# Kernel optimization log

Hardware: AMD Instinct MI355X
Metric: run time of the kernel (lower is better)

The kernel has to match this reference:

```python
import jax, jax.numpy as jnp
import numpy as np

TOP_K = 64
TEMPERATURE = 1.0
EPS = 1e-12  # torch F.normalize eps


def _normalize(v):
    # matches torch.nn.functional.normalize(v, dim=-1)
    n = jnp.linalg.norm(v, axis=-1, keepdims=True)
    return v / jnp.maximum(n, EPS)


def setup_inputs() -> dict:
    key = jax.random.key(0)
    k1, k2 = jax.random.split(key)
    x = jax.random.normal(k1, (4, 1024, 768), dtype=jnp.float32)
    codebook = jax.random.normal(k2, (8192, 768), dtype=jnp.float32)
    alpha = jnp.float32(0.5)
    return {"x": x, "codebook": codebook, "alpha": alpha}


def reference(x, codebook, alpha):
    K = TOP_K
    x_n = _normalize(x)                              # [B,T,D]
    cb_n = _normalize(codebook)                      # [N,D]
    sims = jnp.einsum('btd,nd->btn', x_n, cb_n)      # [B,T,N]
    activations = jax.nn.relu(sims)
    topk_vals, topk_idx = jax.lax.top_k(activations, K)  # [B,T,K]
    protos = codebook[topk_idx]                      # [B,T,K,D] gather
    protos_n = _normalize(protos)
    # per-token KxK pairwise similarity
    sim = jnp.einsum('btkd,btjd->btkj', protos_n, protos_n)
    sim = sim - jnp.eye(K, dtype=sim.dtype)
    sim = jax.nn.relu(sim)
    w = jax.nn.softmax(topk_vals / TEMPERATURE, axis=-1)  # [B,T,K]
    inhibition = jnp.einsum('btkj,btj->btk', sim, w)      # [B,T,K]
    result_topk = jax.nn.relu(topk_vals * (1.0 - alpha * inhibition))
    out = jnp.einsum('btk,btkd->btd', result_topk, protos)  # weighted sum
    return x + out
```

## Files before the change

kernel.cpp:

```cpp
#include <hip/hip_runtime.h>

#define TOKENS 4096
#define DIM    768
#define NCODE  8192
#define TOPK   64
#define CAP    512
#define LCAP   24
#define TAU    0.07f
#define NBIN   256
#define SELCAP 128
#define POOL   80
#define BLO    61
#define BHI    67

typedef __attribute__((ext_vector_type(4))) float          f32x4;
typedef __attribute__((ext_vector_type(8))) _Float16       half8;
typedef __attribute__((ext_vector_type(8))) unsigned short ushort8;

__device__ __forceinline__ unsigned short f2h(float f) {
  _Float16 h = (_Float16)f;
  return *(unsigned short*)&h;
}
__device__ __forceinline__ float h2f(unsigned short u) {
  _Float16 h = *(_Float16*)&u;
  return (float)h;
}

__device__ __forceinline__ int binof(float v) {
  int b = (int)((v - TAU) * (256.0f / 0.28f));
  return b < 0 ? 0 : (b > 255 ? 255 : b);
}

__device__ __forceinline__ void gload16(const unsigned short* g, unsigned short* l) {
  __builtin_amdgcn_global_load_lds((const __attribute__((address_space(1))) unsigned int*)g,
                                   (__attribute__((address_space(3))) unsigned int*)l,
                                   16, 0, 0);
}

__device__ __forceinline__ double dot12(const float4& xa, const float4& xb, const float4& xc,
                                        const float4& a, const float4& b, const float4& c) {
  double acc = (double)xa.x * (double)a.x;
  acc = fma((double)xa.y, (double)a.y, acc);
  acc = fma((double)xa.z, (double)a.z, acc);
  acc = fma((double)xa.w, (double)a.w, acc);
  acc = fma((double)xb.x, (double)b.x, acc);
  acc = fma((double)xb.y, (double)b.y, acc);
  acc = fma((double)xb.z, (double)b.z, acc);
  acc = fma((double)xb.w, (double)b.w, acc);
  acc = fma((double)xc.x, (double)c.x, acc);
  acc = fma((double)xc.y, (double)c.y, acc);
  acc = fma((double)xc.z, (double)c.z, acc);
  acc = fma((double)xc.w, (double)c.w, acc);
  return acc;
}

__global__ __launch_bounds__(256) void normcvt_kernel(const float* __restrict__ V,
                                                      unsigned short* __restrict__ Vn,
                                                      double* __restrict__ Rd) {
  int row = blockIdx.x, tid = threadIdx.x;
  const float* v = V + (size_t)row * DIM;
  float a = v[tid], b = v[tid + 256], c = v[tid + 512];
  double s = (double)a * a + (double)b * b + (double)c * c;
#pragma unroll
  for (int off = 32; off > 0; off >>= 1) s += __shfl_xor(s, off);
  __shared__ double red[4];
  __shared__ float s_rf;
  if ((tid & 63) == 0) red[tid >> 6] = s;
  __syncthreads();
  if (tid == 0) {
    double t = red[0] + red[1] + red[2] + red[3];
    double r = 1.0 / fmax(sqrt(t), 1e-12);
    Rd[row] = r;
    s_rf = (float)r;
  }
  __syncthreads();
  float rf = s_rf;
  unsigned short* o = Vn + (size_t)row * DIM;
  o[tid]       = f2h(a * rf);
  o[tid + 256] = f2h(b * rf);
  o[tid + 512] = f2h(c * rf);
}

__global__ __launch_bounds__(256, 4) void cand_gemm(const unsigned short* __restrict__ Xn,
                                                    const unsigned short* __restrict__ CBn,
                                                    int* __restrict__ cnt,
                                                    float* __restrict__ cval,
                                                    int* __restrict__ cidxg) {
  __shared__ __attribute__((aligned(16))) unsigned short As[2][128 * 32];
  __shared__ __attribute__((aligned(16))) unsigned short Bs[2][128 * 32];
  int tid = threadIdx.x;

  int bid = blockIdx.x;
  int xcd = bid & 7;
  int pos = bid >> 3;
  int sr  = pos >> 6;
  int rr  = pos & 63;
  int mt  = sr * 8 + (rr & 7);
  int nt  = xcd * 8 + (rr >> 3);
  int bm = mt * 128, bn = nt * 128;

  int wave = tid >> 6, lane = tid & 63;
  int wm = (wave >> 1) * 64, wn = (wave & 1) * 64;
  int col = lane & 15, q = lane >> 4;

  const unsigned short* gA0 = Xn  + (size_t)(bm + wave * 32 + (lane >> 2)) * DIM + (lane & 3) * 8;
  const unsigned short* gB0 = CBn + (size_t)(bn + wave * 32 + (lane >> 2)) * DIM + (lane & 3) * 8;
  int lofs = wave * 32 * 32;

  f32x4 acc[4][4];
#pragma unroll
  for (int mi = 0; mi < 4; ++mi)
#pragma unroll
    for (int ni = 0; ni < 4; ++ni) acc[mi][ni] = (f32x4){0.f, 0.f, 0.f, 0.f};

#pragma unroll
  for (int j = 0; j < 2; ++j) {
    gload16(gA0 + (size_t)(j * 16) * DIM, &As[0][lofs + j * 16 * 32]);
    gload16(gB0 + (size_t)(j * 16) * DIM, &Bs[0][lofs + j * 16 * 32]);
  }

  for (int it = 0; it < 24; ++it) {
    int cur = it & 1, nxt = cur ^ 1;
    __syncthreads();
    if (it < 23) {
      int k1 = (it + 1) * 32;
#pragma unroll
      for (int j = 0; j < 2; ++j) {
        gload16(gA0 + (size_t)(j * 16) * DIM + k1, &As[nxt][lofs + j * 16 * 32]);
        gload16(gB0 + (size_t)(j * 16) * DIM + k1, &Bs[nxt][lofs + j * 16 * 32]);
      }
    }
    int ko = q * 8;
    half8 af[4], bf[4];
#pragma unroll
    for (int mi = 0; mi < 4; ++mi)
      af[mi] = *(const half8*)&As[cur][(wm + mi * 16 + col) * 32 + ko];
#pragma unroll
    for (int ni = 0; ni < 4; ++ni)
      bf[ni] = *(const half8*)&Bs[cur][(wn + ni * 16 + col) * 32 + ko];
#pragma unroll
    for (int mi = 0; mi < 4; ++mi)
#pragma unroll
      for (int ni = 0; ni < 4; ++ni)
        acc[mi][ni] = __builtin_amdgcn_mfma_f32_16x16x32_f16(af[mi], bf[ni], acc[mi][ni], 0, 0, 0);
  }
  __syncthreads();

  float* lv            = (float*)&As[0][0];
  unsigned short* lid  = (unsigned short*)&Bs[0][0];
  int* lcnt            = (int*)(&Bs[0][0] + 128 * LCAP);
  int* lbase           = lcnt + 128;
  if (tid < 128) lcnt[tid] = 0;
  __syncthreads();
#pragma unroll
  for (int mi = 0; mi < 4; ++mi)
#pragma unroll
    for (int rg = 0; rg < 4; ++rg) {
      int ml = wm + mi * 16 + q * 4 + rg;
#pragma unroll
      for (int ni = 0; ni < 4; ++ni) {
        float val = acc[mi][ni][rg];
        if (val > TAU) {
          int n = bn + wn + ni * 16 + col;
          int s = atomicAdd(&lcnt[ml], 1);
          if (s < LCAP) { lv[ml * LCAP + s] = val; lid[ml * LCAP + s] = (unsigned short)n; }
        }
      }
    }
  __syncthreads();

  if (tid < 128) {
    int c = lcnt[tid]; c = c < LCAP ? c : LCAP;
    lcnt[tid] = c;
    lbase[tid] = atomicAdd(&cnt[bm + tid], c);
  }
  __syncthreads();
  {
    int ml = tid >> 1, half = tid & 1;
    int c = lcnt[ml], base = lbase[ml], m = bm + ml;
    for (int s = half; s < c; s += 2) {
      int g = base + s;
      if (g < CAP) {
        cval[(size_t)m * CAP + g]  = lv[ml * LCAP + s];
        cidxg[(size_t)m * CAP + g] = (int)lid[ml * LCAP + s];
      }
    }
  }
}

__global__ __launch_bounds__(256) void finale_kernel(const float* __restrict__ X,
                                                     const float* __restrict__ CB,
                                                     const unsigned short* __restrict__ CBn,
                                                     const double* __restrict__ rxd,
                                                     const double* __restrict__ rcd,
                                                     const int* __restrict__ cnt,
                                                     const float* __restrict__ cval,
                                                     const int* __restrict__ cidxg,
                                                     const float* __restrict__ alpha_p,
                                                     float* __restrict__ OUT) {
  int t = blockIdx.x, tid = threadIdx.x;
  int wave = tid >> 6, lane = tid & 63;

  __shared__ __attribute__((aligned(16))) unsigned char u_mem[17408];
  float* s_cv  = (float*)u_mem;
  int*   s_cid = (int*)(u_mem + 2048);
  int*   hist  = (int*)(u_mem + 4096);
  unsigned short (*Pb)[136] = (unsigned short (*)[136])u_mem;

  __shared__ float  sx[DIM];
  __shared__ float  s_selv[SELCAP];
  __shared__ int    s_seli[SELCAP];
  __shared__ float  s_ordv[POOL];
  __shared__ int    s_ord[POOL];
  __shared__ double s_bex[BHI - BLO];
  __shared__ int    s_idx[64];
  __shared__ float  s_vals[64], s_w[64], s_rn[64], s_res[64], s_nrm[64];
  __shared__ int    s_n, s_pivot;

  sx[tid]       = X[(size_t)t * DIM + tid];
  sx[tid + 256] = X[(size_t)t * DIM + tid + 256];
  sx[tid + 512] = X[(size_t)t * DIM + tid + 512];

  int c = cnt[t]; c = c < CAP ? c : CAP;
  for (int s = tid; s < c; s += 256) {
    s_cv[s]  = cval[(size_t)t * CAP + s];
    s_cid[s] = cidxg[(size_t)t * CAP + s];
  }
  hist[tid] = 0;
  if (tid == 0) s_n = 0;
  __syncthreads();
  for (int s = tid; s < c; s += 256) atomicAdd(&hist[binof(s_cv[s])], 1);
  __syncthreads();

  int target = c < POOL ? c : POOL;
  if (wave == 0) {
    int h0 = hist[4 * lane], h1 = hist[4 * lane + 1], h2 = hist[4 * lane + 2], h3 = hist[4 * lane + 3];
    int T = h0 + h1 + h2 + h3;
#pragma unroll
    for (int off = 1; off < 64; off <<= 1) {
      int x = __shfl_down(T, off);
      T += (lane + off < 64) ? x : 0;
    }
    int s0 = T, s1 = T - h0, s2 = s1 - h1, s3 = s2 - h2;
    int bk = -1;
    if (s3 >= target) bk = 3;
    else if (s2 >= target) bk = 2;
    else if (s1 >= target) bk = 1;
    else if (s0 >= target) bk = 0;
    unsigned long long m = __ballot(bk >= 0);
    int hl = 63 - __builtin_clzll(m);
    if (lane == hl) s_pivot = 4 * lane + bk;
  }
  __syncthreads();
  int pivot = s_pivot;
  for (int s = tid; s < c; s += 256) {
    if (binof(s_cv[s]) >= pivot) {
      int p = atomicAdd(&s_n, 1);
      if (p < SELCAP) { s_selv[p] = s_cv[s]; s_seli[p] = s_cid[s]; }
    }
  }
  __syncthreads();
  int nsel = s_n < SELCAP ? s_n : SELCAP;

  if (tid < nsel) {
    float vi = s_selv[tid]; int ci = s_seli[tid];
    int rank = 0;
    for (int j = 0; j < nsel; ++j) {
      float vj = s_selv[j]; int cj = s_seli[j];
      rank += (vj > vi || (vj == vi && cj < ci)) ? 1 : 0;
    }
    if (rank < POOL) { s_ord[rank] = ci; s_ordv[rank] = vi; }
  }
  if (tid < 64) { s_vals[tid] = 0.0f; s_idx[tid] = 0; }
  __syncthreads();

  int nord = nsel < POOL ? nsel : POOL;
  int lo = nord < BLO ? nord : BLO;
  int hi = nord < BHI ? nord : BHI;
  int B  = hi - lo;

  float4 xa = *(const float4*)&sx[4 * lane];
  float4 xb = *(const float4*)&sx[256 + 4 * lane];
  float4 xc = *(const float4*)&sx[512 + 4 * lane];
  double rxt = rxd[t];
  for (int j = wave * 2; j < B; j += 8) {
    int r1ok = (j + 1) < B;
    int gi0 = s_ord[lo + j];
    int gi1 = r1ok ? s_ord[lo + j + 1] : gi0;
    const float* p0 = CB + (size_t)gi0 * DIM;
    const float* p1 = CB + (size_t)gi1 * DIM;
    float4 a0 = *(const float4*)(p0 + 4 * lane);
    float4 b0 = *(const float4*)(p0 + 256 + 4 * lane);
    float4 c0 = *(const float4*)(p0 + 512 + 4 * lane);
    float4 a1 = *(const float4*)(p1 + 4 * lane);
    float4 b1 = *(const float4*)(p1 + 256 + 4 * lane);
    float4 c1 = *(const float4*)(p1 + 512 + 4 * lane);
    double acc0 = dot12(xa, xb, xc, a0, b0, c0);
    double acc1 = dot12(xa, xb, xc, a1, b1, c1);
#pragma unroll
    for (int off = 32; off > 0; off >>= 1) {
      acc0 += __shfl_xor(acc0, off);
      acc1 += __shfl_xor(acc1, off);
    }
    if (lane == 0) {
      double v0 = acc0 * rxt * rcd[gi0];
      s_bex[j] = v0 > 0.0 ? v0 : 0.0;
      if (r1ok) {
        double v1 = acc1 * rxt * rcd[gi1];
        s_bex[j + 1] = v1 > 0.0 ? v1 : 0.0;
      }
    }
  }
  __syncthreads();

  if (tid < lo) { s_idx[tid] = s_ord[tid]; s_vals[tid] = s_ordv[tid]; }
  if (tid < B) {
    double vi = s_bex[tid]; int ci = s_ord[lo + tid];
    int rb = 0;
    for (int j = 0; j < B; ++j) {
      double vj = s_bex[j]; int cj = s_ord[lo + j];
      rb += (vj > vi || (vj == vi && cj < ci)) ? 1 : 0;
    }
    int slot = lo + rb;
    if (slot < TOPK) { s_idx[slot] = ci; s_vals[slot] = (float)vi; }
  }
  __syncthreads();

  if (tid < 64) s_nrm[tid] = (float)(1.0 / rcd[s_idx[tid]]);

  if (tid < 64) {
    float v = s_vals[tid];
    float m = v;
#pragma unroll
    for (int off = 32; off > 0; off >>= 1) m = fmaxf(m, __shfl_xor(m, off));
    float e = expf(v - m);
    float se = e;
#pragma unroll
    for (int off = 32; off > 0; off >>= 1) se += __shfl_xor(se, off);
    s_w[tid] = e / se;
  }

  int q = lane >> 4, col = lane & 15;
  int frow = wave * 16 + col;
  int kof  = q * 8;
  f32x4 gacc[4];
#pragma unroll
  for (int cj = 0; cj < 4; ++cj) gacc[cj] = (f32x4){0.f, 0.f, 0.f, 0.f};
  int r = tid >> 2, qq = tid & 3;
  __syncthreads();
  const unsigned short* Pg = CBn + (size_t)s_idx[r] * DIM;
  ushort8 st[4];
#pragma unroll
  for (int j = 0; j < 4; ++j) st[j] = *(const ushort8*)(Pg + qq * 32 + j * 8);
  for (int cch = 0; cch < 6; ++cch) {
    if (cch) __syncthreads();
#pragma unroll
    for (int j = 0; j < 4; ++j) *(ushort8*)&Pb[r][qq * 32 + j * 8] = st[j];
    if (cch < 5) {
#pragma unroll
      for (int j = 0; j < 4; ++j)
        st[j] = *(const ushort8*)(Pg + (cch + 1) * 128 + qq * 32 + j * 8);
    }
    __syncthreads();
#pragma unroll
    for (int ks = 0; ks < 4; ++ks) {
      half8 a = *(const half8*)&Pb[frow][ks * 32 + kof];
#pragma unroll
      for (int cj = 0; cj < 4; ++cj) {
        half8 b = *(const half8*)&Pb[cj * 16 + col][ks * 32 + kof];
        gacc[cj] = __builtin_amdgcn_mfma_f32_16x16x32_f16(a, b, gacc[cj], 0, 0, 0);
      }
    }
  }

#pragma unroll
  for (int cj = 0; cj < 4; ++cj) {
    if (cj == wave) {
#pragma unroll
      for (int rg = 0; rg < 4; ++rg) {
        if (col == q * 4 + rg)
          s_rn[wave * 16 + q * 4 + rg] =
              1.0f / fmaxf(sqrtf(fmaxf(gacc[cj][rg], 0.0f)), 1e-12f);
      }
    }
  }
  __syncthreads();

  float alpha = alpha_p[0];
  {
    float inh[4] = {0.f, 0.f, 0.f, 0.f};
#pragma unroll
    for (int rg = 0; rg < 4; ++rg) {
      int i = wave * 16 + q * 4 + rg;
      float rni = s_rn[i];
#pragma unroll
      for (int cj = 0; cj < 4; ++cj) {
        int jcol = cj * 16 + col;
        if (jcol != i) {
          float sim = fmaxf(gacc[cj][rg] * rni * s_rn[jcol], 0.0f);
          inh[rg] += sim * s_w[jcol];
        }
      }
    }
#pragma unroll
    for (int off = 1; off < 16; off <<= 1) {
#pragma unroll
      for (int rg = 0; rg < 4; ++rg) inh[rg] += __shfl_xor(inh[rg], off);
    }
    if (col == 0) {
#pragma unroll
      for (int rg = 0; rg < 4; ++rg) {
        int i = wave * 16 + q * 4 + rg;
        float res = s_vals[i] * (1.0f - alpha * inh[rg]);
        s_res[i] = fmaxf(res, 0.0f) * s_nrm[i];
      }
    }
  }
  __syncthreads();

  float* s_o  = (float*)u_mem;
  float* s_p1 = s_o + DIM;
  {
    float o8[8];
#pragma unroll
    for (int j = 0; j < 8; ++j) o8[j] = 0.f;
    int wr = tid / 96, wc = tid - wr * 96;
    if (wr < 2) {
      const int d8 = wc * 8;
#pragma unroll 8
      for (int i = 0; i < 32; ++i) {
        int k = 2 * i + wr;
        float rk = s_res[k];
        const unsigned short* p = CBn + (size_t)s_idx[k] * DIM + d8;
        ushort8 v = *(const ushort8*)p;
#pragma unroll
        for (int j = 0; j < 8; ++j) o8[j] += rk * h2f(v[j]);
      }
    }
    if (wr == 1) {
#pragma unroll
      for (int j = 0; j < 8; ++j) s_p1[wc * 8 + j] = o8[j];
    }
    __syncthreads();
    if (wr == 0) {
#pragma unroll
      for (int j = 0; j < 8; ++j) s_o[wc * 8 + j] = o8[j] + s_p1[wc * 8 + j];
    }
    __syncthreads();
  }

  OUT[(size_t)t * DIM + tid]       = sx[tid]       + s_o[tid];
  OUT[(size_t)t * DIM + tid + 256] = sx[tid + 256] + s_o[tid + 256];
  OUT[(size_t)t * DIM + tid + 512] = sx[tid + 512] + s_o[tid + 512];
}

extern "C" void kernel_launch(void* const* d_in, const int* in_sizes, int n_in,
                              void* d_out, int out_size, void* d_ws, size_t ws_size,
                              hipStream_t stream) {
  const float* X       = (const float*)d_in[0];
  const float* CB      = (const float*)d_in[1];
  const float* alpha_p = (const float*)d_in[2];
  float* OUT = (float*)d_out;

  double* rxd  = (double*)d_ws;
  double* rcd  = rxd + TOKENS;
  int*    cnt  = (int*)(rcd + NCODE);
  float*  cval = (float*)(cnt + TOKENS);
  int*    cidxg= (int*)(cval + (size_t)TOKENS * CAP);
  unsigned short* Xn  = (unsigned short*)(cidxg + (size_t)TOKENS * CAP);
  unsigned short* CBn = Xn + (size_t)TOKENS * DIM;

  hipMemsetAsync(cnt, 0, TOKENS * sizeof(int), stream);
  hipLaunchKernelGGL(normcvt_kernel, dim3(TOKENS), dim3(256), 0, stream, X, Xn, rxd);
  hipLaunchKernelGGL(normcvt_kernel, dim3(NCODE), dim3(256), 0, stream, CB, CBn, rcd);
  hipLaunchKernelGGL(cand_gemm, dim3(2048), dim3(256), 0, stream,
                     Xn, CBn, cnt, cval, cidxg);
  hipLaunchKernelGGL(finale_kernel, dim3(TOKENS), dim3(256), 0, stream,
                     X, CB, CBn, rxd, rcd, cnt, cval, cidxg, alpha_p, OUT);
}
```

Baseline: 281.2 us.

## Quantize normalized codebook to int8 for finale gathers, shrink candidate buffers

Adds a per-row int8 quantization of the normalized codebook, with a scale, inside a single merged normalization launch over tokens and codes. The finale kernel now reads int8 prototypes for both the KxK Gram MFMA staging and the weighted-sum output, which halves gather bandwidth compared with fp16. Candidate indices are stored as ushort, CAP drops from 512 to 384, and x is no longer staged in shared memory but re-read from global. The int8 reconstruction of prototypes lowers accuracy of the output sum and the inhibition term, and the smaller CAP risks dropping candidates.

```diff
diff --git a/kernel.cpp b/kernel.cpp
--- a/kernel.cpp
+++ b/kernel.cpp
@@ -4,7 +4,7 @@
 #define DIM    768
 #define NCODE  8192
 #define TOPK   64
-#define CAP    512
+#define CAP    384
 #define LCAP   24
 #define TAU    0.07f
 #define NBIN   256
@@ -16,6 +16,8 @@
 typedef __attribute__((ext_vector_type(4))) float          f32x4;
 typedef __attribute__((ext_vector_type(8))) _Float16       half8;
 typedef __attribute__((ext_vector_type(8))) unsigned short ushort8;
+typedef __attribute__((ext_vector_type(16))) signed char   c8x16;
+typedef __attribute__((ext_vector_type(8)))  signed char   c8x8;
 
 __device__ __forceinline__ unsigned short f2h(float f) {
   _Float16 h = (_Float16)f;
@@ -54,38 +56,69 @@
   return acc;
 }
 
-__global__ __launch_bounds__(256) void normcvt_kernel(const float* __restrict__ V,
-                                                      unsigned short* __restrict__ Vn,
-                                                      double* __restrict__ Rd) {
+__global__ __launch_bounds__(256) void normcvt_kernel(const float* __restrict__ X,
+                                                      const float* __restrict__ CB,
+                                                      unsigned short* __restrict__ Xn,
+                                                      unsigned short* __restrict__ CBn,
+                                                      signed char* __restrict__ CBq,
+                                                      float* __restrict__ scs,
+                                                      double* __restrict__ rxd,
+                                                      double* __restrict__ rcd) {
   int row = blockIdx.x, tid = threadIdx.x;
-  const float* v = V + (size_t)row * DIM;
+  bool isCB = row >= TOKENS;
+  int lrow = isCB ? row - TOKENS : row;
+  const float* v = (isCB ? CB : X) + (size_t)lrow * DIM;
   float a = v[tid], b = v[tid + 256], c = v[tid + 512];
   double s = (double)a * a + (double)b * b + (double)c * c;
 #pragma unroll
   for (int off = 32; off > 0; off >>= 1) s += __shfl_xor(s, off);
   __shared__ double red[4];
-  __shared__ float s_rf;
+  __shared__ float s_rf, s_qs;
+  __shared__ float redm[4];
   if ((tid & 63) == 0) red[tid >> 6] = s;
   __syncthreads();
   if (tid == 0) {
     double t = red[0] + red[1] + red[2] + red[3];
     double r = 1.0 / fmax(sqrt(t), 1e-12);
-    Rd[row] = r;
+    (isCB ? rcd : rxd)[lrow] = r;
     s_rf = (float)r;
   }
   __syncthreads();
   float rf = s_rf;
-  unsigned short* o = Vn + (size_t)row * DIM;
-  o[tid]       = f2h(a * rf);
-  o[tid + 256] = f2h(b * rf);
-  o[tid + 512] = f2h(c * rf);
+  float na = a * rf, nb = b * rf, nc = c * rf;
+  unsigned short* o = (isCB ? CBn : Xn) + (size_t)lrow * DIM;
+  o[tid]       = f2h(na);
+  o[tid + 256] = f2h(nb);
+  o[tid + 512] = f2h(nc);
+  if (isCB) {
+    float m = fmaxf(fabsf(na), fmaxf(fabsf(nb), fabsf(nc)));
+#pragma unroll
+    for (int off = 32; off > 0; off >>= 1) m = fmaxf(m, __shfl_xor(m, off));
+    if ((tid & 63) == 0) redm[tid >> 6] = m;
+    __syncthreads();
+    if (tid == 0) {
+      float M = fmaxf(fmaxf(redm[0], redm[1]), fmaxf(redm[2], redm[3]));
+      M = fmaxf(M, 1e-8f);
+      s_qs = 127.0f / M;
+      scs[lrow] = M / 127.0f;
+    }
+    __syncthreads();
+    float qs = s_qs;
+    signed char* q = CBq + (size_t)lrow * DIM;
+    int qa = (int)rintf(na * qs); qa = qa > 127 ? 127 : (qa < -127 ? -127 : qa);
+    int qb = (int)rintf(nb * qs); qb = qb > 127 ? 127 : (qb < -127 ? -127 : qb);
+    int qc = (int)rintf(nc * qs); qc = qc > 127 ? 127 : (qc < -127 ? -127 : qc);
+    q[tid]       = (signed char)qa;
+    q[tid + 256] = (signed char)qb;
+    q[tid + 512] = (signed char)qc;
+  }
 }
 
 __global__ __launch_bounds__(256, 4) void cand_gemm(const unsigned short* __restrict__ Xn,
                                                     const unsigned short* __restrict__ CBn,
                                                     int* __restrict__ cnt,
                                                     float* __restrict__ cval,
-                                                    int* __restrict__ cidxg) {
+                                                    unsigned short* __restrict__ cidx) {
   __shared__ __attribute__((aligned(16))) unsigned short As[2][128 * 32];
   __shared__ __attribute__((aligned(16))) unsigned short Bs[2][128 * 32];
   int tid = threadIdx.x;
@@ -148,7 +181,7 @@
 
   float* lv            = (float*)&As[0][0];
   unsigned short* lid  = (unsigned short*)&Bs[0][0];
-  int* lcnt            = (int*)(&Bs[0][0] + 128 * LCAP);
+  int* lcnt            = (int*)((char*)&Bs[0][0] + 128 * LCAP * 2);
   int* lbase           = lcnt + 128;
   if (tid < 128) lcnt[tid] = 0;
   __syncthreads();
@@ -181,8 +214,8 @@
     for (int s = half; s < c; s += 2) {
       int g = base + s;
       if (g < CAP) {
-        cval[(size_t)m * CAP + g]  = lv[ml * LCAP + s];
-        cidxg[(size_t)m * CAP + g] = (int)lid[ml * LCAP + s];
+        cval[(size_t)m * CAP + g] = lv[ml * LCAP + s];
+        cidx[(size_t)m * CAP + g] = lid[ml * LCAP + s];
       }
     }
   }
@@ -190,12 +223,13 @@
 
 __global__ __launch_bounds__(256) void finale_kernel(const float* __restrict__ X,
                                                      const float* __restrict__ CB,
-                                                     const unsigned short* __restrict__ CBn,
+                                                     const signed char* __restrict__ CBq,
+                                                     const float* __restrict__ scs,
                                                      const double* __restrict__ rxd,
                                                      const double* __restrict__ rcd,
                                                      const int* __restrict__ cnt,
                                                      const float* __restrict__ cval,
-                                                     const int* __restrict__ cidxg,
+                                                     const unsigned short* __restrict__ cidx,
                                                      const float* __restrict__ alpha_p,
                                                      float* __restrict__ OUT) {
   int t = blockIdx.x, tid = threadIdx.x;
@@ -207,24 +241,19 @@
   int*   hist  = (int*)(u_mem + 4096);
   unsigned short (*Pb)[136] = (unsigned short (*)[136])u_mem;
 
-  __shared__ float  sx[DIM];
   __shared__ float  s_selv[SELCAP];
   __shared__ int    s_seli[SELCAP];
   __shared__ float  s_ordv[POOL];
   __shared__ int    s_ord[POOL];
   __shared__ double s_bex[BHI - BLO];
   __shared__ int    s_idx[64];
-  __shared__ float  s_vals[64], s_w[64], s_rn[64], s_res[64], s_nrm[64];
+  __shared__ float  s_vals[64], s_w[64], s_rn[64], s_res[64];
   __shared__ int    s_n, s_pivot;
-
-  sx[tid]       = X[(size_t)t * DIM + tid];
-  sx[tid + 256] = X[(size_t)t * DIM + tid + 256];
-  sx[tid + 512] = X[(size_t)t * DIM + tid + 512];
 
   int c = cnt[t]; c = c < CAP ? c : CAP;
   for (int s = tid; s < c; s += 256) {
     s_cv[s]  = cval[(size_t)t * CAP + s];
-    s_cid[s] = cidxg[(size_t)t * CAP + s];
+    s_cid[s] = (int)cidx[(size_t)t * CAP + s];
   }
   hist[tid] = 0;
   if (tid == 0) s_n = 0;
@@ -279,9 +308,9 @@
   int hi = nord < BHI ? nord : BHI;
   int B  = hi - lo;
 
-  float4 xa = *(const float4*)&sx[4 * lane];
-  float4 xb = *(const float4*)&sx[256 + 4 * lane];
-  float4 xc = *(const float4*)&sx[512 + 4 * lane];
+  float4 xa = *(const float4*)(X + (size_t)t * DIM + 4 * lane);
+  float4 xb = *(const float4*)(X + (size_t)t * DIM + 256 + 4 * lane);
+  float4 xc = *(const float4*)(X + (size_t)t * DIM + 512 + 4 * lane);
   double rxt = rxd[t];
   for (int j = wave * 2; j < B; j += 8) {
     int r1ok = (j + 1) < B;
@@ -326,8 +355,6 @@
   }
   __syncthreads();
 
-  if (tid < 64) s_nrm[tid] = (float)(1.0 / rcd[s_idx[tid]]);
-
   if (tid < 64) {
     float v = s_vals[tid];
     float m = v;
@@ -348,18 +375,22 @@
   for (int cj = 0; cj < 4; ++cj) gacc[cj] = (f32x4){0.f, 0.f, 0.f, 0.f};
   int r = tid >> 2, qq = tid & 3;
   __syncthreads();
-  const unsigned short* Pg = CBn + (size_t)s_idx[r] * DIM;
-  ushort8 st[4];
-#pragma unroll
-  for (int j = 0; j < 4; ++j) st[j] = *(const ushort8*)(Pg + qq * 32 + j * 8);
+  const signed char* Pg = CBq + (size_t)s_idx[r] * DIM;
+  c8x16 stq[2];
+  stq[0] = *(const c8x16*)(Pg + qq * 32);
+  stq[1] = *(const c8x16*)(Pg + qq * 32 + 16);
   for (int cch = 0; cch < 6; ++cch) {
     if (cch) __syncthreads();
 #pragma unroll
-    for (int j = 0; j < 4; ++j) *(ushort8*)&Pb[r][qq * 32 + j * 8] = st[j];
+    for (int j = 0; j < 4; ++j) {
+      ushort8 w;
+#pragma unroll
+      for (int e = 0; e < 8; ++e) w[e] = f2h((float)stq[j >> 1][(j & 1) * 8 + e]);
+      *(ushort8*)&Pb[r][qq * 32 + j * 8] = w;
+    }
     if (cch < 5) {
-#pragma unroll
-      for (int j = 0; j < 4; ++j)
-        st[j] = *(const ushort8*)(Pg + (cch + 1) * 128 + qq * 32 + j * 8);
+      stq[0] = *(const c8x16*)(Pg + (cch + 1) * 128 + qq * 32);
+      stq[1] = *(const c8x16*)(Pg + (cch + 1) * 128 + qq * 32 + 16);
     }
     __syncthreads();
 #pragma unroll
@@ -411,8 +442,9 @@
 #pragma unroll
       for (int rg = 0; rg < 4; ++rg) {
         int i = wave * 16 + q * 4 + rg;
+        int gi = s_idx[i];
         float res = s_vals[i] * (1.0f - alpha * inh[rg]);
-        s_res[i] = fmaxf(res, 0.0f) * s_nrm[i];
+        s_res[i] = fmaxf(res, 0.0f) * scs[gi] * (float)(1.0 / rcd[gi]);
       }
     }
   }
@@ -431,10 +463,10 @@
       for (int i = 0; i < 32; ++i) {
         int k = 2 * i + wr;
         float rk = s_res[k];
-        const unsigned short* p = CBn + (size_t)s_idx[k] * DIM + d8;
-        ushort8 v = *(const ushort8*)p;
-#pragma unroll
-        for (int j = 0; j < 8; ++j) o8[j] += rk * h2f(v[j]);
+        const signed char* p = CBq + (size_t)s_idx[k] * DIM + d8;
+        c8x8 v = *(const c8x8*)p;
+#pragma unroll
+        for (int j = 0; j < 8; ++j) o8[j] += rk * (float)v[j];
       }
     }
     if (wr == 1) {
@@ -449,9 +481,9 @@
     __syncthreads();
   }
 
-  OUT[(size_t)t * DIM + tid]       = sx[tid]       + s_o[tid];
-  OUT[(size_t)t * DIM + tid + 256] = sx[tid + 256] + s_o[tid + 256];
-  OUT[(size_t)t * DIM + tid + 512] = sx[tid + 512] + s_o[tid + 512];
+  OUT[(size_t)t * DIM + tid]       = X[(size_t)t * DIM + tid]       + s_o[tid];
+  OUT[(size_t)t * DIM + tid + 256] = X[(size_t)t * DIM + tid + 256] + s_o[tid + 256];
+  OUT[(size_t)t * DIM + tid + 512] = X[(size_t)t * DIM + tid + 512] + s_o[tid + 512];
 }
 
 extern "C" void kernel_launch(void* const* d_in, const int* in_sizes, int n_in,
@@ -462,19 +494,21 @@
   const float* alpha_p = (const float*)d_in[2];
   float* OUT = (float*)d_out;
 
-  double* rxd  = (double*)d_ws;
-  double* rcd  = rxd + TOKENS;
-  int*    cnt  = (int*)(rcd + NCODE);
-  float*  cval = (float*)(cnt + TOKENS);
-  int*    cidxg= (int*)(cval + (size_t)TOKENS * CAP);
-  unsigned short* Xn  = (unsigned short*)(cidxg + (size_t)TOKENS * CAP);
-  unsigned short* CBn = Xn + (size_t)TOKENS * DIM;
+  double* rxd          = (double*)d_ws;
+  double* rcd          = rxd + TOKENS;
+  int*    cnt          = (int*)(rcd + NCODE);
+  float*  cval         = (float*)(cnt + TOKENS);
+  unsigned short* cidx = (unsigned short*)(cval + (size_t)TOKENS * CAP);
+  unsigned short* Xn   = cidx + (size_t)TOKENS * CAP;
+  unsigned short* CBn  = Xn + (size_t)TOKENS * DIM;
+  signed char*    CBq  = (signed char*)(CBn + (size_t)NCODE * DIM);
+  float*          scs  = (float*)(CBq + (size_t)NCODE * DIM);
 
   hipMemsetAsync(cnt, 0, TOKENS * sizeof(int), stream);
-  hipLaunchKernelGGL(normcvt_kernel, dim3(TOKENS), dim3(256), 0, stream, X, Xn, rxd);
-  hipLaunchKernelGGL(normcvt_kernel, dim3(NCODE), dim3(256), 0, stream, CB, CBn, rcd);
+  hipLaunchKernelGGL(normcvt_kernel, dim3(TOKENS + NCODE), dim3(256), 0, stream,
+                     X, CB, Xn, CBn, CBq, scs, rxd, rcd);
   hipLaunchKernelGGL(cand_gemm, dim3(2048), dim3(256), 0, stream,
-                     Xn, CBn, cnt, cval, cidxg);
+                     Xn, CBn, cnt, cval, cidx);
   hipLaunchKernelGGL(finale_kernel, dim3(TOKENS), dim3(256), 0, stream,
-                     X, CB, CBn, rxd, rcd, cnt, cval, cidxg, alpha_p, OUT);
-}
+                     X, CB, CBq, scs, rxd, rcd, cnt, cval, cidx, alpha_p, OUT);
+}
```

New measurement: 275.2 us. 2.1% less time.
